# Performance work log

Measured on AMD Instinct MI355X. Metric: run time of the kernel, lower is better.

Reference implementation:

```python
import jax, jax.numpy as jnp
import numpy as np

HEADS, DIM_HEAD = 8, 64  # per init_kwargs


def cdist(x, w):
    """Euclidean distance between rows of x [..., n, d] and w [m, d] -> [..., n, m].
    Matches torch.cdist (non-squared) / L2DistanceLinear(squared=False)."""
    sq = (x * x).sum(-1, keepdims=True) + (w * w).sum(-1) - 2.0 * (x @ w.T)
    return jnp.sqrt(jnp.maximum(sq, 0.0))


def setup_inputs() -> dict:
    key = jax.random.key(0)
    k1, k2, k3 = jax.random.split(key, 3)
    B, N, D = 4, 2048, 512
    dim_inner = HEADS * DIM_HEAD  # 512
    x = jax.random.normal(k1, (B, N, D), dtype=jnp.float32)
    w_qkv = jax.random.normal(k2, (3 * dim_inner, D), dtype=jnp.float32)
    w_out = jax.random.normal(k3, (D, dim_inner), dtype=jnp.float32)
    return {"x": x, "w_qkv": w_qkv, "w_out": w_out}


def reference(x, w_qkv, w_out):
    B, N, D = x.shape
    scale = DIM_HEAD ** -0.5

    # L2-distance QKV projection (cdist, non-squared, no negate/bias)
    qkv = cdist(x, w_qkv)                                  # [B, N, 3*H*DH]
    qkv = qkv.reshape(B, N, 3, HEADS, DIM_HEAD).transpose(2, 0, 3, 1, 4)  # [3, B, H, N, DH]
    q, k, v = qkv[0], qkv[1], qkv[2]

    # neg squared-L2 attention scores: -(||q||^2 + ||k||^2 - 2 q.k)
    q_sq = (q * q).sum(-1)                                 # [B, H, N]
    k_sq = (k * k).sum(-1)                                 # [B, H, N]
    dots = jnp.einsum('bhid,bhjd->bhij', q, k)             # [B, H, N, N]
    sim = -(q_sq[..., :, None] + k_sq[..., None, :] - 2.0 * dots) * scale

    attn = jax.nn.softmax(sim, axis=-1)
    out = jnp.einsum('bhij,bhjd->bhid', attn, v)           # [B, H, N, DH]
    out = out.transpose(0, 2, 1, 3).reshape(B, N, HEADS * DIM_HEAD)

    # L2-distance output projection
    return cdist(out, w_out)                               # [B, N, D]
```

## Files before the change

kernel.cpp:

```cpp
#include <hip/hip_runtime.h>
#include <stdint.h>

typedef float v4f  __attribute__((ext_vector_type(4)));
typedef float v16f __attribute__((ext_vector_type(16)));
typedef short v8s  __attribute__((ext_vector_type(8)));
typedef uint32_t u32;

#define DEVI static __device__ __forceinline__

DEVI unsigned short f2bf(float f) {
    u32 u = __builtin_bit_cast(u32, f);
    u = (u + 0x7fffu + ((u >> 16) & 1u)) >> 16;
    return (unsigned short)u;
}
DEVI float bf2f(unsigned short h) {
    u32 u = ((u32)h) << 16;
    return __builtin_bit_cast(float, u);
}

template <typename T>
DEVI void async16(const T* g, T* l) {
    __builtin_amdgcn_global_load_lds(
        (const __attribute__((address_space(1))) u32*)g,
        (__attribute__((address_space(3))) u32*)l, 16, 0, 0);
}

DEVI v4f bmfma(v8s a, v8s b, v4f c) {
    return __builtin_amdgcn_mfma_f32_16x16x32_bf16(a, b, c, 0, 0, 0);
}
DEVI v16f bmfma32(v8s a, v8s b, v16f c) {
    return __builtin_amdgcn_mfma_f32_32x32x16_bf16(a, b, c, 0, 0, 0);
}

static const size_t HSZ = 32ull * 2048 * 64;

__launch_bounds__(256, 2)
__global__ void prep_rows(const float* __restrict__ X, unsigned short* __restrict__ Xb,
                          float* __restrict__ Sq, float* __restrict__ Rs, int hasRs)
{
    const int w = threadIdx.x >> 6, lane = threadIdx.x & 63;
    const int r = blockIdx.x * 4 + w;
    const float* xr = X + (size_t)r * 512 + lane * 8;
    float4 a = *(const float4*)xr;
    float4 c = *(const float4*)(xr + 4);
    float s = a.x*a.x + a.y*a.y + a.z*a.z + a.w*a.w
            + c.x*c.x + c.y*c.y + c.z*c.z + c.w*c.w;
    float sm = a.x + a.y + a.z + a.w + c.x + c.y + c.z + c.w;
    uint4 pkv;
    unsigned short* e = (unsigned short*)&pkv;
    e[0] = f2bf(a.x); e[1] = f2bf(a.y); e[2] = f2bf(a.z); e[3] = f2bf(a.w);
    e[4] = f2bf(c.x); e[5] = f2bf(c.y); e[6] = f2bf(c.z); e[7] = f2bf(c.w);
    *(uint4*)(Xb + (size_t)r * 512 + lane * 8) = pkv;
#pragma unroll
    for (int d = 32; d > 0; d >>= 1) {
        s  += __shfl_xor(s, d);
        sm += __shfl_xor(sm, d);
    }
    if (lane == 0) { Sq[r] = s; if (hasRs) Rs[r] = sm; }
}

__launch_bounds__(256, 2)
__global__ void outsq_kernel(const unsigned short* __restrict__ Op, float* __restrict__ Osq)
{
    const int w = threadIdx.x >> 6, lane = threadIdx.x & 63;
    const int r = blockIdx.x * 4 + w;
    uint4 pk = *(const uint4*)(Op + (size_t)r * 512 + lane * 8);
    const unsigned short* e = (const unsigned short*)&pk;
    float s = 0.f;
#pragma unroll
    for (int u = 0; u < 8; ++u) { float f = bf2f(e[u]) + 32.f; s += f * f; }
#pragma unroll
    for (int d = 32; d > 0; d >>= 1) s += __shfl_xor(s, d);
    if (lane == 0) Osq[r] = s;
}

__launch_bounds__(256, 2)
__global__ void gemm_cdist(const unsigned short* __restrict__ A,
                           const unsigned short* __restrict__ B,
                           const float* __restrict__ Asq,
                           const float* __restrict__ Bsq,
                           unsigned short* __restrict__ QKV,
                           float* __restrict__ Ksqc)
{
    __shared__ unsigned short lsm[2 * 128 * 64];
    unsigned short* lA = lsm;
    unsigned short* lB = lsm + 128 * 64;
    const int t = threadIdx.x;
    const int lane = t & 63, w = t >> 6;
    const int low = lane & 15, quad = lane >> 4;
    const int wm = w & 1, wn = w >> 1;
    const int tM = blockIdx.x * 128, tN = blockIdx.y * 128;

    v4f acc[4][4];
#pragma unroll
    for (int a = 0; a < 4; ++a)
#pragma unroll
        for (int b = 0; b < 4; ++b) acc[a][b] = (v4f){0.f, 0.f, 0.f, 0.f};

    for (int kt = 0; kt < 512; kt += 64) {
        __syncthreads();
#pragma unroll
        for (int is = 0; is < 4; ++is) {
            int slot = is * 256 + t;
            int r = slot >> 3, bp = slot & 7;
            int bs = bp ^ (r & 7);
            async16(A + (size_t)(tM + r) * 512 + kt + bs * 8, lA + slot * 8);
            async16(B + (size_t)(tN + r) * 512 + kt + bs * 8, lB + slot * 8);
        }
        __syncthreads();

        v8s bfr[4][2];
#pragma unroll
        for (int ns = 0; ns < 4; ++ns) {
            int row = wn * 64 + ns * 16 + low;
#pragma unroll
            for (int kc = 0; kc < 2; ++kc)
                bfr[ns][kc] = *(const v8s*)(lB + (row * 8 + ((kc * 4 + quad) ^ (row & 7))) * 8);
        }
#pragma unroll
        for (int ms = 0; ms < 4; ++ms) {
            int row = wm * 64 + ms * 16 + low;
            v8s af0 = *(const v8s*)(lA + (row * 8 + ((0 + quad) ^ (row & 7))) * 8);
            v8s af1 = *(const v8s*)(lA + (row * 8 + ((4 + quad) ^ (row & 7))) * 8);
#pragma unroll
            for (int ns = 0; ns < 4; ++ns) {
                acc[ms][ns] = bmfma(af0, bfr[ns][0], acc[ms][ns]);
                acc[ms][ns] = bmfma(af1, bfr[ns][1], acc[ms][ns]);
            }
        }
    }

    const int tt = tN >> 9;
    if (tt != 2) {
#pragma unroll
        for (int ms = 0; ms < 4; ++ms) {
#pragma unroll
            for (int reg = 0; reg < 4; ++reg) {
                const int row = tM + wm * 64 + ms * 16 + quad * 4 + reg;
                const int b = row >> 11, i = row & 2047;
                float kacc = 0.f;
#pragma unroll
                for (int ns = 0; ns < 4; ++ns) {
                    const int col = tN + wn * 64 + ns * 16 + low;
                    float dot = acc[ms][ns][reg];
                    float val = sqrtf(fmaxf(Asq[row] + Bsq[col] - 2.f * dot, 0.f)) - 32.f;
                    int h = (col >> 6) & 7, d = col & 63, bh = b * 8 + h;
                    if (tt == 0) {
                        QKV[((size_t)bh * 2048 + i) * 64 + d] =
                            f2bf(val * 0.36067376022224085f);
                    } else {
                        QKV[HSZ + ((size_t)bh * 2048 + i) * 64 + d] = f2bf(val);
                        kacc += val * val;
                    }
                }
                if (tt == 1) {
#pragma unroll
                    for (int d = 1; d < 16; d <<= 1) kacc += __shfl_xor(kacc, d);
                    if (low == 0) {
                        int h = ((tN + wn * 64) >> 6) & 7;
                        Ksqc[(size_t)(b * 8 + h) * 2048 + i] = kacc * 0.18033688011112042f;
                    }
                }
            }
        }
    } else {
        u32 packed[4][4][2];
#pragma unroll
        for (int ms = 0; ms < 4; ++ms)
#pragma unroll
            for (int ns = 0; ns < 4; ++ns) {
                const int col = tN + wn * 64 + ns * 16 + low;
                float bs_ = Bsq[col];
#pragma unroll
                for (int rp = 0; rp < 2; ++rp) {
                    u32 pk = 0;
#pragma unroll
                    for (int sub = 0; sub < 2; ++sub) {
                        int reg = rp * 2 + sub;
                        int row = tM + wm * 64 + ms * 16 + quad * 4 + reg;
                        float val = sqrtf(fmaxf(Asq[row] + bs_
                                                - 2.f * acc[ms][ns][reg], 0.f)) - 32.f;
                        pk |= (u32)f2bf(val) << (16 * sub);
                    }
                    packed[ms][ns][rp] = pk;
                }
            }
        u32* lT32 = (u32*)lsm;
#pragma unroll
        for (int p = 0; p < 2; ++p) {
            __syncthreads();
            if (wm == p) {
#pragma unroll
                for (int ms = 0; ms < 4; ++ms)
#pragma unroll
                    for (int ns = 0; ns < 4; ++ns) {
                        int cl = wn * 64 + ns * 16 + low;
#pragma unroll
                        for (int rp = 0; rp < 2; ++rp)
                            lT32[cl * 36 + ms * 8 + quad * 2 + rp] = packed[ms][ns][rp];
                    }
            }
            __syncthreads();
#pragma unroll
            for (int cc = 0; cc < 4; ++cc) {
                int col = cc * 32 + (t >> 3);
                int i0 = (t & 7) * 8;
                uint4 vvv = *(const uint4*)(lsm + col * 72 + i0);
                int colg = tN + col;
                int h = (colg >> 6) & 7, d = colg & 63;
                int rowg = tM + p * 64 + i0;
                int b = rowg >> 11, i = rowg & 2047;
                *(uint4*)(QKV + 2 * HSZ
                          + ((size_t)((b * 8 + h) * 64 + d)) * 2048 + i) = vvv;
            }
        }
    }
}

__launch_bounds__(256, 3)
__global__ void flash_attn(const unsigned short* __restrict__ Q,
                           const unsigned short* __restrict__ K,
                           const unsigned short* __restrict__ VT,
                           const float* __restrict__ Ksqc,
                           unsigned short* __restrict__ PO,
                           float* __restrict__ PL)
{
    __shared__ unsigned short lK[64 * 64];
    __shared__ unsigned short lV[64 * 64];
    __shared__ float lKq[64];
    const int t = threadIdx.x, lane = t & 63, w = t >> 6;
    const int i31 = lane & 31, h = lane >> 5;
    const int qt = blockIdx.x, bh = blockIdx.y, sp = blockIdx.z;
    const size_t base = (size_t)bh * (2048 * 64);
    const int row0 = qt * 128 + w * 32;
    const int j0 = sp * 1024;

    v8s qfr[4];
#pragma unroll
    for (int kt = 0; kt < 4; ++kt)
        qfr[kt] = *(const v8s*)(Q + base + (size_t)(row0 + i31) * 64 + kt * 16 + h * 8);

    float nmq;
    {
        float s = 0.f;
#pragma unroll
        for (int kt = 0; kt < 4; ++kt) {
            const unsigned short* qe = (const unsigned short*)&qfr[kt];
#pragma unroll
            for (int u = 0; u < 8; ++u) { float f = bf2f(qe[u]); s += f * f; }
        }
        s += __shfl_xor(s, 32);
        nmq = -s * 1.3862943611198906f;
    }

    v16f o[2];
    float lacc = 0.f;
#pragma unroll
    for (int dt = 0; dt < 2; ++dt)
#pragma unroll
        for (int r = 0; r < 16; ++r) o[dt][r] = 0.f;

    const unsigned short* kg = K + base + (size_t)j0 * 64;
    const unsigned short* vg = VT + (size_t)bh * 64 * 2048 + j0;
    const float* kqg = Ksqc + (size_t)bh * 2048 + j0;

    for (int iter = 0; iter < 16; ++iter) {
        __syncthreads();
#pragma unroll
        for (int is = 0; is < 2; ++is) {
            int slot = is * 256 + t;
            int r = slot >> 3, bp = slot & 7, bs = bp ^ (r & 7);
            async16(kg + (size_t)r * 64 + bs * 8, lK + slot * 8);
        }
#pragma unroll
        for (int is = 0; is < 2; ++is) {
            int slot = is * 256 + t;
            int r = slot >> 3, bp = slot & 7, bs = bp ^ (r & 7);
            async16(vg + (size_t)r * 2048 + bs * 8, lV + slot * 8);
        }
        if (t < 16) async16(kqg + t * 4, lKq + t * 4);
        __syncthreads();
        kg += 64 * 64; vg += 64; kqg += 64;

#pragma unroll
        for (int T = 0; T < 2; ++T) {
            const int jrow = T * 32 + i31;
            v8s kf[4];
#pragma unroll
            for (int kt = 0; kt < 4; ++kt)
                kf[kt] = *(const v8s*)(lK + (jrow * 8 + ((2 * kt + h) ^ (jrow & 7))) * 8);
            v4f kqv[4];
#pragma unroll
            for (int r1 = 0; r1 < 4; ++r1)
                kqv[r1] = *(const v4f*)(lKq + T * 32 + r1 * 8 + h * 4);

            v16f sa;
#pragma unroll
            for (int r = 0; r < 16; ++r) sa[r] = nmq - kqv[r >> 2][r & 3];
#pragma unroll
            for (int kt = 0; kt < 4; ++kt)
                sa = bmfma32(kf[kt], qfr[kt], sa);

            float p[16];
            float ls = 0.f;
#pragma unroll
            for (int r = 0; r < 16; ++r) { p[r] = exp2f(sa[r]); ls += p[r]; }
            lacc += ls;
            u32 pk[8];
#pragma unroll
            for (int r1 = 0; r1 < 4; ++r1) {
                pk[2 * r1] = __builtin_amdgcn_perm(
                    __builtin_bit_cast(u32, p[4 * r1 + 1]),
                    __builtin_bit_cast(u32, p[4 * r1 + 0]), 0x07060302u);
                pk[2 * r1 + 1] = __builtin_amdgcn_perm(
                    __builtin_bit_cast(u32, p[4 * r1 + 3]),
                    __builtin_bit_cast(u32, p[4 * r1 + 2]), 0x07060302u);
            }

#pragma unroll
            for (int c2 = 0; c2 < 2; ++c2) {
                const int jb = 2 * (2 * T + c2);
                u32 pa0 = pk[4 * c2 + 0], pa1 = pk[4 * c2 + 1];
                u32 pb0 = pk[4 * c2 + 2], pb1 = pk[4 * c2 + 3];
                u32 own0 = h ? pb0 : pa0, own1 = h ? pb1 : pa1;
                u32 snd0 = h ? pa0 : pb0, snd1 = h ? pa1 : pb1;
                u32 rcv0 = __shfl_xor(snd0, 32);
                u32 rcv1 = __shfl_xor(snd1, 32);
                uint4 dd;
                dd.x = h ? rcv0 : own0; dd.y = h ? rcv1 : own1;
                dd.z = h ? own0 : rcv0; dd.w = h ? own1 : rcv1;
                v8s af = __builtin_bit_cast(v8s, dd);
#pragma unroll
                for (int dt = 0; dt < 2; ++dt) {
                    const int drow = dt * 32 + i31;
                    v8s vf = *(const v8s*)(lV + (drow * 8 + ((jb + h) ^ (drow & 7))) * 8);
                    o[dt] = bmfma32(af, vf, o[dt]);
                }
            }
        }
    }

    const int pb = (qt * 32 + bh) * 2 + sp;
    unsigned short* pob = PO + (size_t)pb * 8192;
    lacc += __shfl_xor(lacc, 32);
#pragma unroll
    for (int dt = 0; dt < 2; ++dt)
#pragma unroll
        for (int r = 0; r < 16; ++r) {
            int rl = w * 32 + (r & 3) + 8 * (r >> 2) + 4 * h;
            pob[rl * 64 + dt * 32 + i31] = f2bf(o[dt][r]);
        }
    if (h == 0)
        PL[(size_t)pb * 128 + w * 32 + i31] = lacc;
}

__launch_bounds__(256, 2)
__global__ void combine_kernel(const unsigned short* __restrict__ PO,
                               const float* __restrict__ PL,
                               unsigned short* __restrict__ O)
{
    const int bx = blockIdx.x, bh = blockIdx.y, t = threadIdx.x;
    const int b = bh >> 3, h = bh & 7;
    const int gi = bx * 64 + (t >> 2);
    const int qt = gi >> 7, rl = gi & 127;
    const int pbase = (qt * 32 + bh) * 2;
    const int c0 = (t & 3) * 16;
    float lsum = PL[(size_t)pbase * 128 + rl] + PL[(size_t)(pbase + 1) * 128 + rl];
    float inv = 1.f / lsum;
    float accv[16];
#pragma unroll
    for (int u = 0; u < 16; ++u) accv[u] = 0.f;
    const unsigned short* a = PO + (size_t)pbase * 8192 + rl * 64 + c0;
#pragma unroll
    for (int s = 0; s < 2; ++s) {
        uint4 a0 = *(const uint4*)(a + (size_t)s * 8192);
        uint4 a1 = *(const uint4*)(a + (size_t)s * 8192 + 8);
        const unsigned short* ae = (const unsigned short*)&a0;
#pragma unroll
        for (int u = 0; u < 8; ++u) accv[u] += bf2f(ae[u]);
        ae = (const unsigned short*)&a1;
#pragma unroll
        for (int u = 0; u < 8; ++u) accv[8 + u] += bf2f(ae[u]);
    }
    uint4 o0, o1;
    unsigned short* oe = (unsigned short*)&o0;
#pragma unroll
    for (int u = 0; u < 8; ++u) oe[u] = f2bf(accv[u] * inv);
    oe = (unsigned short*)&o1;
#pragma unroll
    for (int u = 0; u < 8; ++u) oe[u] = f2bf(accv[8 + u] * inv);
    unsigned short* dst = O + ((size_t)(b * 2048 + gi)) * 512 + h * 64 + c0;
    *(uint4*)dst = o0;
    *(uint4*)(dst + 8) = o1;
}

__launch_bounds__(256, 2)
__global__ void gemm_out(const unsigned short* __restrict__ A,
                         const unsigned short* __restrict__ B,
                         const float* __restrict__ Asq,
                         const float* __restrict__ Bsq,
                         const float* __restrict__ Brs,
                         float* __restrict__ OUT)
{
    __shared__ unsigned short lA[128 * 64];
    __shared__ unsigned short lB[64 * 64];
    const int t = threadIdx.x;
    const int lane = t & 63, w = t >> 6;
    const int low = lane & 15, quad = lane >> 4;
    const int wm = w & 1, wn = w >> 1;
    const int tM = blockIdx.x * 128, tN = blockIdx.y * 64;

    v4f acc[4][2];
#pragma unroll
    for (int a = 0; a < 4; ++a)
#pragma unroll
        for (int b = 0; b < 2; ++b) acc[a][b] = (v4f){0.f, 0.f, 0.f, 0.f};

    for (int kt = 0; kt < 512; kt += 64) {
        __syncthreads();
#pragma unroll
        for (int is = 0; is < 4; ++is) {
            int slot = is * 256 + t;
            int r = slot >> 3, bp = slot & 7, bs = bp ^ (r & 7);
            async16(A + (size_t)(tM + r) * 512 + kt + bs * 8, lA + slot * 8);
        }
#pragma unroll
        for (int is = 0; is < 2; ++is) {
            int slot = is * 256 + t;
            int r = slot >> 3, bp = slot & 7, bs = bp ^ (r & 7);
            async16(B + (size_t)(tN + r) * 512 + kt + bs * 8, lB + slot * 8);
        }
        __syncthreads();

        v8s bfr[2][2];
#pragma unroll
        for (int ns = 0; ns < 2; ++ns) {
            int row = wn * 32 + ns * 16 + low;
#pragma unroll
            for (int kc = 0; kc < 2; ++kc)
                bfr[ns][kc] = *(const v8s*)(lB + (row * 8 + ((kc * 4 + quad) ^ (row & 7))) * 8);
        }
#pragma unroll
        for (int ms = 0; ms < 4; ++ms) {
            int row = wm * 64 + ms * 16 + low;
            v8s af0 = *(const v8s*)(lA + (row * 8 + ((0 + quad) ^ (row & 7))) * 8);
            v8s af1 = *(const v8s*)(lA + (row * 8 + ((4 + quad) ^ (row & 7))) * 8);
#pragma unroll
            for (int ns = 0; ns < 2; ++ns) {
                acc[ms][ns] = bmfma(af0, bfr[ns][0], acc[ms][ns]);
                acc[ms][ns] = bmfma(af1, bfr[ns][1], acc[ms][ns]);
            }
        }
    }

#pragma unroll
    for (int ms = 0; ms < 4; ++ms) {
#pragma unroll
        for (int ns = 0; ns < 2; ++ns) {
#pragma unroll
            for (int reg = 0; reg < 4; ++reg) {
                int row = tM + wm * 64 + ms * 16 + quad * 4 + reg;
                int col = tN + wn * 32 + ns * 16 + low;
                float val = sqrtf(fmaxf(Asq[row] + Bsq[col]
                                        - 2.f * (acc[ms][ns][reg] + 32.f * Brs[col]), 0.f));
                OUT[(size_t)row * 512 + col] = val;
            }
        }
    }
}

extern "C" void kernel_launch(void* const* d_in, const int* in_sizes, int n_in,
                              void* d_out, int out_size, void* d_ws, size_t ws_size,
                              hipStream_t stream)
{
    const float* x    = (const float*)d_in[0];
    const float* wqkv = (const float*)d_in[1];
    const float* wout = (const float*)d_in[2];
    float* out = (float*)d_out;

    char* ws = (char*)d_ws;
    size_t off = 0;
    auto alloc = [&](size_t bytes) -> void* {
        void* p = ws + off;
        off += (bytes + 255) & ~(size_t)255;
        return p;
    };
    unsigned short* xb   = (unsigned short*)alloc(8192ull * 512 * 2);
    unsigned short* wqb  = (unsigned short*)alloc(1536ull * 512 * 2);
    unsigned short* wob  = (unsigned short*)alloc(512ull * 512 * 2);
    unsigned short* qkv  = (unsigned short*)alloc(3ull * HSZ * 2);
    unsigned short* outp = (unsigned short*)alloc(8192ull * 512 * 2);
    unsigned short* po   = (unsigned short*)alloc(1024ull * 8192 * 2);
    float* pl   = (float*)alloc(1024ull * 128 * 4);
    float* xsq  = (float*)alloc(8192 * 4);
    float* wqsq = (float*)alloc(1536 * 4);
    float* wosq = (float*)alloc(512 * 4);
    float* wors = (float*)alloc(512 * 4);
    float* ksqc = (float*)alloc(65536ull * 4);
    float* osq  = (float*)alloc(8192 * 4);

    prep_rows<<<2048, 256, 0, stream>>>(x, xb, xsq, nullptr, 0);
    prep_rows<<<384, 256, 0, stream>>>(wqkv, wqb, wqsq, nullptr, 0);
    prep_rows<<<128, 256, 0, stream>>>(wout, wob, wosq, wors, 1);

    gemm_cdist<<<dim3(64, 12), 256, 0, stream>>>(xb, wqb, xsq, wqsq, qkv, ksqc);
    flash_attn<<<dim3(16, 32, 2), 256, 0, stream>>>(qkv, qkv + HSZ, qkv + 2 * HSZ,
                                                    ksqc, po, pl);
    combine_kernel<<<dim3(32, 32), 256, 0, stream>>>(po, pl, outp);
    outsq_kernel<<<2048, 256, 0, stream>>>(outp, osq);
    gemm_out<<<dim3(64, 8), 256, 0, stream>>>(outp, wob, osq, wosq, wors, out);
}
```

Measured before the change: 190.9 us.

## Double-buffer flash attention K/V tiles and fuse prep and combine kernels

Flash attention now keeps two LDS buffers for K, V and the K-norm vector, so the next tile's async loads are issued while the current tile is computed, and one barrier per iteration is removed. The P fragment exchange through cross-lane shuffles is replaced by reading V in a permuted layout that matches the packed P registers. The three row-prep launches are merged into one kernel, and the combine kernel now also computes the output row squared norms, which removes the separate outsq pass. LDS use in attention doubles, which may reduce occupancy at 3 blocks per CU, and the V reads become two 8-byte loads instead of one 16-byte load.

```diff
diff --git a/kernel.cpp b/kernel.cpp
--- a/kernel.cpp
+++ b/kernel.cpp
@@ -35,11 +35,20 @@
 static const size_t HSZ = 32ull * 2048 * 64;
 
 __launch_bounds__(256, 2)
-__global__ void prep_rows(const float* __restrict__ X, unsigned short* __restrict__ Xb,
-                          float* __restrict__ Sq, float* __restrict__ Rs, int hasRs)
+__global__ void prep_all(const float* __restrict__ x, const float* __restrict__ wqkv,
+                         const float* __restrict__ wout,
+                         unsigned short* __restrict__ xb, unsigned short* __restrict__ wqb,
+                         unsigned short* __restrict__ wob,
+                         float* __restrict__ xsq, float* __restrict__ wqsq,
+                         float* __restrict__ wosq, float* __restrict__ wors)
 {
+    const int bid = blockIdx.x;
     const int w = threadIdx.x >> 6, lane = threadIdx.x & 63;
-    const int r = blockIdx.x * 4 + w;
+    const float* X; unsigned short* Xb; float* Sq; float* Rs = nullptr; int r0;
+    if (bid < 2048)      { X = x;    Xb = xb;  Sq = xsq;  r0 = bid * 4; }
+    else if (bid < 2432) { X = wqkv; Xb = wqb; Sq = wqsq; r0 = (bid - 2048) * 4; }
+    else                 { X = wout; Xb = wob; Sq = wosq; Rs = wors; r0 = (bid - 2432) * 4; }
+    const int r = r0 + w;
     const float* xr = X + (size_t)r * 512 + lane * 8;
     float4 a = *(const float4*)xr;
     float4 c = *(const float4*)(xr + 4);
@@ -56,22 +65,7 @@
         s  += __shfl_xor(s, d);
         sm += __shfl_xor(sm, d);
     }
-    if (lane == 0) { Sq[r] = s; if (hasRs) Rs[r] = sm; }
-}
-
-__launch_bounds__(256, 2)
-__global__ void outsq_kernel(const unsigned short* __restrict__ Op, float* __restrict__ Osq)
-{
-    const int w = threadIdx.x >> 6, lane = threadIdx.x & 63;
-    const int r = blockIdx.x * 4 + w;
-    uint4 pk = *(const uint4*)(Op + (size_t)r * 512 + lane * 8);
-    const unsigned short* e = (const unsigned short*)&pk;
-    float s = 0.f;
-#pragma unroll
-    for (int u = 0; u < 8; ++u) { float f = bf2f(e[u]) + 32.f; s += f * f; }
-#pragma unroll
-    for (int d = 32; d > 0; d >>= 1) s += __shfl_xor(s, d);
-    if (lane == 0) Osq[r] = s;
+    if (lane == 0) { Sq[r] = s; if (Rs) Rs[r] = sm; }
 }
 
 __launch_bounds__(256, 2)
@@ -225,9 +219,9 @@
                            unsigned short* __restrict__ PO,
                            float* __restrict__ PL)
 {
-    __shared__ unsigned short lK[64 * 64];
-    __shared__ unsigned short lV[64 * 64];
-    __shared__ float lKq[64];
+    __shared__ unsigned short lK[2][64 * 64];
+    __shared__ unsigned short lV[2][64 * 64];
+    __shared__ __align__(16) float lKq[2][64];
     const int t = threadIdx.x, lane = t & 63, w = t >> 6;
     const int i31 = lane & 31, h = lane >> 5;
     const int qt = blockIdx.x, bh = blockIdx.y, sp = blockIdx.z;
@@ -264,23 +258,31 @@
     const unsigned short* vg = VT + (size_t)bh * 64 * 2048 + j0;
     const float* kqg = Ksqc + (size_t)bh * 2048 + j0;
 
-    for (int iter = 0; iter < 16; ++iter) {
-        __syncthreads();
+    auto stage = [&](int buf) {
 #pragma unroll
         for (int is = 0; is < 2; ++is) {
             int slot = is * 256 + t;
             int r = slot >> 3, bp = slot & 7, bs = bp ^ (r & 7);
-            async16(kg + (size_t)r * 64 + bs * 8, lK + slot * 8);
+            async16(kg + (size_t)r * 64 + bs * 8, &lK[buf][slot * 8]);
         }
 #pragma unroll
         for (int is = 0; is < 2; ++is) {
             int slot = is * 256 + t;
             int r = slot >> 3, bp = slot & 7, bs = bp ^ (r & 7);
-            async16(vg + (size_t)r * 2048 + bs * 8, lV + slot * 8);
-        }
-        if (t < 16) async16(kqg + t * 4, lKq + t * 4);
+            async16(vg + (size_t)r * 2048 + bs * 8, &lV[buf][slot * 8]);
+        }
+        if (t < 16) async16(kqg + t * 4, &lKq[buf][t * 4]);
+        kg += 64 * 64; vg += 64; kqg += 64;
+    };
+
+    stage(0);
+    int cur = 0;
+    for (int iter = 0; iter < 16; ++iter) {
         __syncthreads();
-        kg += 64 * 64; vg += 64; kqg += 64;
+        if (iter < 15) stage(cur ^ 1);
+        const unsigned short* lKc = lK[cur];
+        const unsigned short* lVc = lV[cur];
+        const float* lKqc = lKq[cur];
 
 #pragma unroll
         for (int T = 0; T < 2; ++T) {
@@ -288,11 +290,11 @@
             v8s kf[4];
 #pragma unroll
             for (int kt = 0; kt < 4; ++kt)
-                kf[kt] = *(const v8s*)(lK + (jrow * 8 + ((2 * kt + h) ^ (jrow & 7))) * 8);
+                kf[kt] = *(const v8s*)(lKc + (jrow * 8 + ((2 * kt + h) ^ (jrow & 7))) * 8);
             v4f kqv[4];
 #pragma unroll
             for (int r1 = 0; r1 < 4; ++r1)
-                kqv[r1] = *(const v4f*)(lKq + T * 32 + r1 * 8 + h * 4);
+                kqv[r1] = *(const v4f*)(lKqc + T * 32 + r1 * 8 + h * 4);
 
             v16f sa;
 #pragma unroll
@@ -319,25 +321,24 @@
 
 #pragma unroll
             for (int c2 = 0; c2 < 2; ++c2) {
-                const int jb = 2 * (2 * T + c2);
-                u32 pa0 = pk[4 * c2 + 0], pa1 = pk[4 * c2 + 1];
-                u32 pb0 = pk[4 * c2 + 2], pb1 = pk[4 * c2 + 3];
-                u32 own0 = h ? pb0 : pa0, own1 = h ? pb1 : pa1;
-                u32 snd0 = h ? pa0 : pb0, snd1 = h ? pa1 : pb1;
-                u32 rcv0 = __shfl_xor(snd0, 32);
-                u32 rcv1 = __shfl_xor(snd1, 32);
-                uint4 dd;
-                dd.x = h ? rcv0 : own0; dd.y = h ? rcv1 : own1;
-                dd.z = h ? own0 : rcv0; dd.w = h ? own1 : rcv1;
-                v8s af = __builtin_bit_cast(v8s, dd);
+                uint4 au;
+                au.x = pk[4 * c2 + 0]; au.y = pk[4 * c2 + 1];
+                au.z = pk[4 * c2 + 2]; au.w = pk[4 * c2 + 3];
+                v8s af = __builtin_bit_cast(v8s, au);
+                const int b0 = 4 * T + 2 * c2;
 #pragma unroll
                 for (int dt = 0; dt < 2; ++dt) {
                     const int drow = dt * 32 + i31;
-                    v8s vf = *(const v8s*)(lV + (drow * 8 + ((jb + h) ^ (drow & 7))) * 8);
-                    o[dt] = bmfma32(af, vf, o[dt]);
+                    const unsigned short* vrow = lVc + drow * 64;
+                    const int s7 = drow & 7;
+                    uint2 lo = *(const uint2*)(vrow + (((b0    ) ^ s7) << 3) + h * 4);
+                    uint2 hi = *(const uint2*)(vrow + (((b0 + 1) ^ s7) << 3) + h * 4);
+                    uint4 vv; vv.x = lo.x; vv.y = lo.y; vv.z = hi.x; vv.w = hi.y;
+                    o[dt] = bmfma32(af, __builtin_bit_cast(v8s, vv), o[dt]);
                 }
             }
         }
+        cur ^= 1;
     }
 
     const int pb = (qt * 32 + bh) * 2 + sp;
@@ -355,43 +356,42 @@
 }
 
 __launch_bounds__(256, 2)
-__global__ void combine_kernel(const unsigned short* __restrict__ PO,
-                               const float* __restrict__ PL,
-                               unsigned short* __restrict__ O)
+__global__ void combine_osq(const unsigned short* __restrict__ PO,
+                            const float* __restrict__ PL,
+                            unsigned short* __restrict__ O,
+                            float* __restrict__ Osq)
 {
-    const int bx = blockIdx.x, bh = blockIdx.y, t = threadIdx.x;
-    const int b = bh >> 3, h = bh & 7;
-    const int gi = bx * 64 + (t >> 2);
-    const int qt = gi >> 7, rl = gi & 127;
-    const int pbase = (qt * 32 + bh) * 2;
-    const int c0 = (t & 3) * 16;
-    float lsum = PL[(size_t)pbase * 128 + rl] + PL[(size_t)(pbase + 1) * 128 + rl];
+    const int bx = blockIdx.x, b = blockIdx.y, t = threadIdx.x;
+    const int rl = t >> 3, h = t & 7;
+    const int gi = bx * 32 + rl;
+    const int qt = gi >> 7, qrl = gi & 127;
+    const int pbase = (qt * 32 + b * 8 + h) * 2;
+    float lsum = PL[(size_t)pbase * 128 + qrl] + PL[(size_t)(pbase + 1) * 128 + qrl];
     float inv = 1.f / lsum;
-    float accv[16];
-#pragma unroll
-    for (int u = 0; u < 16; ++u) accv[u] = 0.f;
-    const unsigned short* a = PO + (size_t)pbase * 8192 + rl * 64 + c0;
-#pragma unroll
-    for (int s = 0; s < 2; ++s) {
-        uint4 a0 = *(const uint4*)(a + (size_t)s * 8192);
-        uint4 a1 = *(const uint4*)(a + (size_t)s * 8192 + 8);
-        const unsigned short* ae = (const unsigned short*)&a0;
-#pragma unroll
-        for (int u = 0; u < 8; ++u) accv[u] += bf2f(ae[u]);
-        ae = (const unsigned short*)&a1;
-#pragma unroll
-        for (int u = 0; u < 8; ++u) accv[8 + u] += bf2f(ae[u]);
-    }
-    uint4 o0, o1;
-    unsigned short* oe = (unsigned short*)&o0;
-#pragma unroll
-    for (int u = 0; u < 8; ++u) oe[u] = f2bf(accv[u] * inv);
-    oe = (unsigned short*)&o1;
-#pragma unroll
-    for (int u = 0; u < 8; ++u) oe[u] = f2bf(accv[8 + u] * inv);
-    unsigned short* dst = O + ((size_t)(b * 2048 + gi)) * 512 + h * 64 + c0;
-    *(uint4*)dst = o0;
-    *(uint4*)(dst + 8) = o1;
+    const unsigned short* a = PO + (size_t)pbase * 8192 + qrl * 64;
+    unsigned short* dst = O + ((size_t)(b * 2048 + gi)) * 512 + h * 64;
+    float osum = 0.f;
+#pragma unroll
+    for (int c = 0; c < 8; ++c) {
+        uint4 a0 = *(const uint4*)(a + c * 8);
+        uint4 a1 = *(const uint4*)(a + 8192 + c * 8);
+        const unsigned short* e0 = (const unsigned short*)&a0;
+        const unsigned short* e1 = (const unsigned short*)&a1;
+        uint4 ov;
+        unsigned short* oe = (unsigned short*)&ov;
+#pragma unroll
+        for (int u = 0; u < 8; ++u) {
+            unsigned short pb16 = f2bf((bf2f(e0[u]) + bf2f(e1[u])) * inv);
+            oe[u] = pb16;
+            float vv = bf2f(pb16) + 32.f;
+            osum += vv * vv;
+        }
+        *(uint4*)(dst + c * 8) = ov;
+    }
+    osum += __shfl_xor(osum, 1);
+    osum += __shfl_xor(osum, 2);
+    osum += __shfl_xor(osum, 4);
+    if (h == 0) Osq[b * 2048 + gi] = osum;
 }
 
 __launch_bounds__(256, 2)
@@ -499,14 +499,11 @@
     float* ksqc = (float*)alloc(65536ull * 4);
     float* osq  = (float*)alloc(8192 * 4);
 
-    prep_rows<<<2048, 256, 0, stream>>>(x, xb, xsq, nullptr, 0);
-    prep_rows<<<384, 256, 0, stream>>>(wqkv, wqb, wqsq, nullptr, 0);
-    prep_rows<<<128, 256, 0, stream>>>(wout, wob, wosq, wors, 1);
-
+    prep_all<<<2560, 256, 0, stream>>>(x, wqkv, wout, xb, wqb, wob,
+                                       xsq, wqsq, wosq, wors);
     gemm_cdist<<<dim3(64, 12), 256, 0, stream>>>(xb, wqb, xsq, wqsq, qkv, ksqc);
     flash_attn<<<dim3(16, 32, 2), 256, 0, stream>>>(qkv, qkv + HSZ, qkv + 2 * HSZ,
                                                     ksqc, po, pl);
-    combine_kernel<<<dim3(32, 32), 256, 0, stream>>>(po, pl, outp);
-    outsq_kernel<<<2048, 256, 0, stream>>>(outp, osq);
+    combine_osq<<<dim3(64, 4), 256, 0, stream>>>(po, pl, outp, osq);
     gemm_out<<<dim3(64, 8), 256, 0, stream>>>(outp, wob, osq, wosq, wors, out);
 }
```

Measured after the change: 192.4 us. Within noise of the previous version (+0.8%).
